# Performance work log

Hardware: AMD Instinct MI355X
Metric: run time of the kernel (lower is better)

Reference implementation:

```python
import jax, jax.numpy as jnp
import numpy as np

B, L, D_IN, D_MODEL, D_OUT, N_LAYERS, N2 = 16, 2048, 512, 512, 512, 4, 32
Q_STEP = 1.0 / 64.0
LN_EPS = 1e-5


def setup_inputs() -> dict:
    key = jax.random.key(0)
    ks = jax.random.split(key, 12)
    H = D_MODEL
    x = jax.random.normal(ks[0], (B, D_IN, L), jnp.float32)
    # sigma-delta dense encoder / decoder weights (ANN-equivalent: dense + ReLU)
    W_enc = jax.random.normal(ks[1], (H, D_IN), jnp.float32) * (1.0 / np.sqrt(D_IN))
    W_dec = jax.random.normal(ks[2], (D_OUT, H), jnp.float32) * (1.0 / np.sqrt(H))
    # S4D kernel params, stacked over layers. S4D-Lin init.
    log_dt = (jax.random.uniform(ks[3], (N_LAYERS, H), jnp.float32)
              * (np.log(0.1) - np.log(0.001)) + np.log(0.001))
    log_A_real = jnp.full((N_LAYERS, H, N2), np.log(0.5), jnp.float32)
    A_imag = jnp.tile((np.pi * jnp.arange(N2, dtype=jnp.float32))[None, None, :],
                      (N_LAYERS, H, 1))
    C_re = jax.random.normal(ks[4], (N_LAYERS, H, N2), jnp.float32) * (0.5 ** 0.5)
    C_im = jax.random.normal(ks[5], (N_LAYERS, H, N2), jnp.float32) * (0.5 ** 0.5)
    D = jax.random.normal(ks[6], (N_LAYERS, H), jnp.float32)
    # output linear of each S4D block: 1x1 conv H -> 2H followed by GLU
    W_out = jax.random.normal(ks[7], (N_LAYERS, 2 * H, H), jnp.float32) * (1.0 / np.sqrt(H))
    b_out = jnp.zeros((N_LAYERS, 2 * H), jnp.float32)
    ln_g = jnp.ones((N_LAYERS, H), jnp.float32)
    ln_b = jnp.zeros((N_LAYERS, H), jnp.float32)
    return {"x": x, "W_enc": W_enc, "W_dec": W_dec, "log_dt": log_dt,
            "log_A_real": log_A_real, "A_imag": A_imag, "C_re": C_re,
            "C_im": C_im, "D": D, "W_out": W_out, "b_out": b_out,
            "ln_g": ln_g, "ln_b": ln_b}


def _quantize_ste(x, step):
    q = jnp.round(x / step) * step
    return x + jax.lax.stop_gradient(q - x)


def reference(x, W_enc, W_dec, log_dt, log_A_real, A_imag, C_re, C_im, D,
              W_out, b_out, ln_g, ln_b):
    # x: (B, d_input, L) channel-time layout (slayer convention)
    xq = _quantize_ste(x, Q_STEP)
    h = jax.nn.relu(jnp.einsum('bct,dc->bdt', xq, W_enc))  # encoder (B,H,L)
    Lx = h.shape[-1]
    t = jnp.arange(Lx)
    for i in range(N_LAYERS):
        # ---- S4D kernel (ZOH-style discretization) ----
        dt = jnp.exp(log_dt[i])[:, None]                 # (H,1)
        A = -jnp.exp(log_A_real[i]) + 1j * A_imag[i]     # (H,N)
        dtA = dt * A                                     # (H,N)
        Cc = (C_re[i] + 1j * C_im[i]) * jnp.expm1(dtA) / A
        vand = jnp.exp(dtA[:, :, None] * t)              # (H,N,L)
        K = 2.0 * jnp.einsum('hn,hnl->hl', Cc, vand).real  # (H,L)
        # ---- FFT convolution ----
        k_f = jnp.fft.rfft(K, n=2 * Lx)                  # (H, L+1)
        u_f = jnp.fft.rfft(h, n=2 * Lx)                  # (B,H,L+1)
        y = jnp.fft.irfft(u_f * k_f[None], n=2 * Lx)[..., :Lx]
        y = y + D[i][:, None] * h                        # skip connection
        y = jax.nn.gelu(y, approximate=False)
        # output linear: 1x1 conv H->2H + GLU over channel dim
        z = jnp.einsum('bht,dh->bdt', y, W_out[i]) + b_out[i][None, :, None]
        z = z[:, :D_MODEL] * jax.nn.sigmoid(z[:, D_MODEL:])
        # residual + post-norm (LayerNorm over channel dim)
        h = z + h
        mu = h.mean(axis=1, keepdims=True)
        var = h.var(axis=1, keepdims=True)
        h = (h - mu) / jnp.sqrt(var + LN_EPS) * ln_g[i][:, None] + ln_b[i][:, None]
    out = jax.nn.relu(jnp.einsum('bht,dh->bdt', h, W_dec))  # decoder (B,d_out,L)
    return out
```

## Files before the change

kernel.cpp:

```cpp
#include <hip/hip_runtime.h>
#include <cstdint>
#include <cstddef>

typedef __attribute__((ext_vector_type(8))) short short8;
typedef __attribute__((ext_vector_type(8))) _Float16 half8;
typedef __attribute__((ext_vector_type(4))) float floatx4;
typedef __attribute__((ext_vector_type(4))) int intx4;
typedef __attribute__((ext_vector_type(4))) unsigned short ushort4v;

__device__ __forceinline__ unsigned short f2h(float f) {
    union { _Float16 h; unsigned short u; } v;
    v.h = (_Float16)f;
    return v.u;
}
__device__ __forceinline__ float relu_keepnan(float v) {
    return v > 0.f ? v : (v == v ? 0.f : v);
}

__global__ __launch_bounds__(256) void k_cvt(
    const float* __restrict__ src, unsigned short* __restrict__ dst, int n) {
    int i = blockIdx.x * 256 + threadIdx.x;
    if (i < n) dst[i] = f2h(src[i]);
}

__global__ __launch_bounds__(256) void k_precompute(
    const float* __restrict__ ldt, const float* __restrict__ lar,
    const float* __restrict__ aim, const float* __restrict__ cre,
    const float* __restrict__ cim, float4* __restrict__ lwc,
    float2* __restrict__ wt) {
    int idx = blockIdx.x * 256 + threadIdx.x;
    int i = idx >> 14;
    int h = (idx >> 5) & 511;
    int n = idx & 31;
    float dt = expf(ldt[i * 512 + h]);
    float Are = -expf(lar[idx]);
    float Aim = aim[idx];
    float dre = dt * Are, dim = dt * Aim;
    float e = expf(dre);
    float wre = e * cosf(dim);
    float wim = e * sinf(dim);
    float emr = wre - 1.f, emi = wim;
    float inv = 1.f / (Are * Are + Aim * Aim);
    float fr = (emr * Are + emi * Aim) * inv;
    float fi = (emi * Are - emr * Aim) * inv;
    float cr = cre[idx], ci = cim[idx];
    float4 o;
    o.x = wre; o.y = wim;
    o.z = 2.f * (cr * fr - ci * fi);
    o.w = 2.f * (cr * fi + ci * fr);
    int oidx = (i * 32 + n) * 512 + h;
    lwc[oidx] = o;
    float ar = wre, ai = wim;
#pragma unroll
    for (int k = 0; k < 7; ++k) {
        float nr = ar * ar - ai * ai;
        float ni = 2.f * ar * ai;
        ar = nr; ai = ni;
    }
    wt[oidx] = make_float2(ar, ai);
}

__global__ __launch_bounds__(256) void k_quant_transpose(
    const float* __restrict__ x, unsigned short* __restrict__ xq, int b0) {
    __shared__ unsigned short tile[64][65];
    const int bg = b0 + blockIdx.z, bl = blockIdx.z;
    const int c0 = blockIdx.y * 64, t0 = blockIdx.x * 64;
    const int tid = threadIdx.x;
#pragma unroll
    for (int it = 0; it < 16; ++it) {
        int idx = it * 256 + tid;
        int r = idx >> 6, cc = idx & 63;
        float f = x[(size_t)(bg * 512 + c0 + r) * 2048 + t0 + cc];
        float q = rintf(f * 64.f) * 0.015625f;
        tile[r][cc] = f2h(q);
    }
    __syncthreads();
#pragma unroll
    for (int it = 0; it < 16; ++it) {
        int idx = it * 256 + tid;
        int r = idx >> 6, cc = idx & 63;
        xq[(size_t)(bl * 2048 + t0 + r) * 512 + c0 + cc] = tile[cc][r];
    }
}

__global__ __launch_bounds__(256) void k_hf2ut(
    const float* __restrict__ hf, unsigned short* __restrict__ ut, int J) {
    __shared__ unsigned short tile[64][65];
    const int j0 = blockIdx.x * 64, c0 = blockIdx.y * 64;
    const int tid = threadIdx.x;
#pragma unroll
    for (int it = 0; it < 16; ++it) {
        int idx = it * 256 + tid;
        int r = idx >> 6, cc = idx & 63;
        tile[r][cc] = f2h(hf[(size_t)(j0 + r) * 512 + c0 + cc]);
    }
    __syncthreads();
#pragma unroll
    for (int it = 0; it < 16; ++it) {
        int idx = it * 256 + tid;
        int r = idx >> 6, cc = idx & 63;
        ut[(size_t)(c0 + r) * J + j0 + cc] = tile[cc][r];
    }
}

__global__ __launch_bounds__(64) void k_build_wa(
    const float4* __restrict__ lwc, unsigned short* __restrict__ WA, int layer) {
    __shared__ unsigned short Ws[64 * 136];
    const int h = blockIdx.x, tid = threadIdx.x;
    if (tid < 32) {
        float4 v = lwc[((size_t)layer * 32 + tid) * 512 + h];
        float pr = 1.f, pi = 0.f;
        for (int m = 0; m < 128; ++m) {
            Ws[(2 * tid) * 136 + (127 - m)] = f2h(pr);
            Ws[(2 * tid + 1) * 136 + (127 - m)] = f2h(pi);
            float nr = pr * v.x - pi * v.y;
            float ni = pr * v.y + pi * v.x;
            pr = nr; pi = ni;
        }
    }
    __syncthreads();
#pragma unroll
    for (int it = 0; it < 16; ++it) {
        int idx = it * 64 + tid;
        int r = idx >> 4, c8 = idx & 15;
        *(intx4*)(WA + (size_t)h * 8192 + r * 128 + c8 * 8) =
            *(const intx4*)(Ws + r * 136 + c8 * 8);
    }
}

__global__ __launch_bounds__(256) void k_build_T(
    const float4* __restrict__ lwc, const float* __restrict__ Dp,
    unsigned short* __restrict__ TT, int layer) {
    __shared__ float Kvs[128];
    __shared__ unsigned short Mxs[128 * 64];
    __shared__ float wr_s[32], wi_s[32], cr_s[32], ci_s[32];
    const int h = blockIdx.x, tid = threadIdx.x;
    if (tid < 32) {
        float4 v = lwc[((size_t)layer * 32 + tid) * 512 + h];
        wr_s[tid] = v.x; wi_s[tid] = v.y; cr_s[tid] = v.z; ci_s[tid] = v.w;
    }
    __syncthreads();
    if (tid < 32) {
        const int n = tid;
        float wre = wr_s[n], wim = wi_s[n];
        float ar = cr_s[n], ai = ci_s[n];
        for (int m = 0; m <= 128; ++m) {
            if (m < 128) {
                float s = ar;
#pragma unroll
                for (int d = 16; d >= 1; d >>= 1) s += __shfl_xor(s, d, 64);
                if (n == 0) Kvs[m] = s;
            }
            if (m >= 1) {
                Mxs[(m - 1) * 64 + 2 * n] = f2h(ar);
                Mxs[(m - 1) * 64 + 2 * n + 1] = f2h(-ai);
            }
            float nr = ar * wre - ai * wim;
            float ni = ar * wim + ai * wre;
            ar = nr; ai = ni;
        }
    }
    __syncthreads();
    const float Dh = Dp[layer * 512 + h];
#pragma unroll
    for (int it = 0; it < 12; ++it) {
        int idx = it * 256 + tid;
        int t = idx / 24, c8 = idx % 24;
        short8 pack;
#pragma unroll
        for (int q = 0; q < 8; ++q) {
            int k = c8 * 8 + q;
            unsigned short us;
            if (k < 128) {
                float val = (k <= t) ? (Kvs[t - k] + (k == t ? Dh : 0.f)) : 0.f;
                us = f2h(val);
            } else {
                us = Mxs[t * 64 + (k - 128)];
            }
            pack[q] = (short)us;
        }
        *(short8*)(TT + (size_t)h * 24576 + t * 192 + c8 * 8) = pack;
    }
}

template <int MODE>
__global__ __launch_bounds__(256, 2) void k_gemm(
    const unsigned short* __restrict__ A, const unsigned short* __restrict__ Bm,
    float* __restrict__ of32, int b0) {
    __shared__ __align__(16) unsigned short Al[128 * 72];
    __shared__ __align__(16) unsigned short Bl[128 * 72];
    const int tid = threadIdx.x;
    const int m0 = blockIdx.x * 128;
    const int j0 = blockIdx.y * 128;
    const int sub = tid & 7;
    const int row = tid >> 3;
    const unsigned short* Ag = A + (size_t)(m0 + row) * 512 + sub * 8;
    const unsigned short* Bg = Bm + (size_t)(j0 + row) * 512 + sub * 8;
    intx4 ra[4], rb[4];
#pragma unroll
    for (int i = 0; i < 4; ++i) {
        ra[i] = *(const intx4*)(Ag + (size_t)i * 32 * 512);
        rb[i] = *(const intx4*)(Bg + (size_t)i * 32 * 512);
    }
    const int lane = tid & 63;
    const int w = tid >> 6;
    const int wm = w & 1, wn = w >> 1;
    const int l15 = lane & 15, quad = lane >> 4;
    floatx4 acc[4][4] = {};
    for (int kt = 0; kt < 8; ++kt) {
#pragma unroll
        for (int i = 0; i < 4; ++i) {
            *(intx4*)(Al + (row + 32 * i) * 72 + sub * 8) = ra[i];
            *(intx4*)(Bl + (row + 32 * i) * 72 + sub * 8) = rb[i];
        }
        __syncthreads();
        if (kt < 7) {
#pragma unroll
            for (int i = 0; i < 4; ++i) {
                ra[i] = *(const intx4*)(Ag + (size_t)i * 32 * 512 + (kt + 1) * 64);
                rb[i] = *(const intx4*)(Bg + (size_t)i * 32 * 512 + (kt + 1) * 64);
            }
        }
#pragma unroll
        for (int ks = 0; ks < 2; ++ks) {
            half8 af[4], bfr[4];
#pragma unroll
            for (int mt = 0; mt < 4; ++mt)
                af[mt] = *(const half8*)(Al + (wm * 64 + mt * 16 + l15) * 72 + ks * 32 + quad * 8);
#pragma unroll
            for (int nt = 0; nt < 4; ++nt)
                bfr[nt] = *(const half8*)(Bl + (wn * 64 + nt * 16 + l15) * 72 + ks * 32 + quad * 8);
#pragma unroll
            for (int mt = 0; mt < 4; ++mt)
#pragma unroll
                for (int nt = 0; nt < 4; ++nt)
                    acc[mt][nt] = __builtin_amdgcn_mfma_f32_16x16x32_f16(
                        af[mt], bfr[nt], acc[mt][nt], 0, 0, 0);
        }
        __syncthreads();
    }
#pragma unroll
    for (int mt = 0; mt < 4; ++mt) {
#pragma unroll
        for (int nt = 0; nt < 4; ++nt) {
            const int d = m0 + wm * 64 + mt * 16 + quad * 4;
            const int j = j0 + wn * 64 + nt * 16 + l15;
            floatx4 v = acc[mt][nt];
            if (MODE == 0) {
#pragma unroll
                for (int r = 0; r < 4; ++r) v[r] = relu_keepnan(v[r]);
                *(floatx4*)(of32 + (size_t)j * 512 + d) = v;
            } else {
                const int bl = j >> 11, t = j & 2047;
#pragma unroll
                for (int r = 0; r < 4; ++r)
                    of32[((size_t)((b0 + bl) * 512 + d + r)) * 2048 + t] = relu_keepnan(v[r]);
            }
        }
    }
}

__global__ __launch_bounds__(256, 4) void k_stateA(
    const unsigned short* __restrict__ WA, const unsigned short* __restrict__ ut,
    float* __restrict__ P, int J, int Rtot) {
    __shared__ __align__(16) unsigned short Aw[64 * 72];
    __shared__ __align__(16) unsigned short Bw[128 * 72];
    const int tid = threadIdx.x;
    const int h = blockIdx.y;
    const int r0 = blockIdx.x * 128;
    const int sub = tid & 7, row = tid >> 3;
    const unsigned short* Ag = WA + (size_t)h * 8192 + row * 128 + sub * 8;
    const unsigned short* Bg = ut + (size_t)h * J + (size_t)(r0 + row) * 128 + sub * 8;
    intx4 ra[2], rb[4];
    ra[0] = *(const intx4*)(Ag);
    ra[1] = *(const intx4*)(Ag + 32 * 128);
#pragma unroll
    for (int i = 0; i < 4; ++i) rb[i] = *(const intx4*)(Bg + i * 32 * 128);
    const int lane = tid & 63, w = tid >> 6;
    const int wm = w & 1, wn = w >> 1;
    const int l15 = lane & 15, quad = lane >> 4;
    floatx4 acc[2][4] = {};
    for (int kt = 0; kt < 2; ++kt) {
        *(intx4*)(Aw + row * 72 + sub * 8) = ra[0];
        *(intx4*)(Aw + (row + 32) * 72 + sub * 8) = ra[1];
#pragma unroll
        for (int i = 0; i < 4; ++i)
            *(intx4*)(Bw + (row + 32 * i) * 72 + sub * 8) = rb[i];
        __syncthreads();
        if (kt == 0) {
            ra[0] = *(const intx4*)(Ag + 64);
            ra[1] = *(const intx4*)(Ag + 32 * 128 + 64);
#pragma unroll
            for (int i = 0; i < 4; ++i) rb[i] = *(const intx4*)(Bg + i * 32 * 128 + 64);
        }
#pragma unroll
        for (int ks = 0; ks < 2; ++ks) {
            half8 af[2], bfr[4];
#pragma unroll
            for (int mt = 0; mt < 2; ++mt)
                af[mt] = *(const half8*)(Aw + (wm * 32 + mt * 16 + l15) * 72 + ks * 32 + quad * 8);
#pragma unroll
            for (int nt = 0; nt < 4; ++nt)
                bfr[nt] = *(const half8*)(Bw + (wn * 64 + nt * 16 + l15) * 72 + ks * 32 + quad * 8);
#pragma unroll
            for (int mt = 0; mt < 2; ++mt)
#pragma unroll
                for (int nt = 0; nt < 4; ++nt)
                    acc[mt][nt] = __builtin_amdgcn_mfma_f32_16x16x32_f16(
                        af[mt], bfr[nt], acc[mt][nt], 0, 0, 0);
        }
        __syncthreads();
    }
#pragma unroll
    for (int mt = 0; mt < 2; ++mt)
#pragma unroll
        for (int nt = 0; nt < 4; ++nt)
#pragma unroll
            for (int r = 0; r < 4; ++r)
                P[((size_t)h * 64 + wm * 32 + mt * 16 + quad * 4 + r) * Rtot +
                  r0 + wn * 64 + nt * 16 + l15] = acc[mt][nt][r];
}

__global__ __launch_bounds__(64) void k_comb(
    const float* __restrict__ P, const float2* __restrict__ wt,
    unsigned short* __restrict__ S0, int layer, int Rtot) {
    __shared__ float Ps[64][17];
    __shared__ unsigned short S0s[16][64];
    const int h = blockIdx.x, bl = blockIdx.y;
    const int tid = threadIdx.x;
#pragma unroll
    for (int it = 0; it < 4; ++it) {
        int idx = it * 64 + tid;
        int n2 = idx >> 2, pt = idx & 3;
        float4 v = *(const float4*)(P + ((size_t)h * 64 + n2) * Rtot + bl * 16 + pt * 4);
        Ps[n2][pt * 4 + 0] = v.x; Ps[n2][pt * 4 + 1] = v.y;
        Ps[n2][pt * 4 + 2] = v.z; Ps[n2][pt * 4 + 3] = v.w;
    }
    __syncthreads();
    if (tid < 32) {
        const int n = tid;
        float2 wv = wt[((size_t)layer * 32 + n) * 512 + h];
        float ar = 0.f, ai = 0.f;
        for (int g = 0; g < 16; ++g) {
            S0s[g][2 * n] = f2h(ar);
            S0s[g][2 * n + 1] = f2h(ai);
            float pr = Ps[2 * n][g], pi = Ps[2 * n + 1][g];
            float nr = fmaf(wv.x, ar, fmaf(-wv.y, ai, pr));
            float ni = fmaf(wv.x, ai, fmaf(wv.y, ar, pi));
            ar = nr; ai = ni;
        }
    }
    __syncthreads();
    const int g = tid >> 2, pt = tid & 3;
    unsigned short* dst = S0 + ((size_t)h * Rtot + bl * 16 + g) * 64 + pt * 16;
    *(intx4*)(dst) = *(const intx4*)(&S0s[g][pt * 16]);
    *(intx4*)(dst + 8) = *(const intx4*)(&S0s[g][pt * 16 + 8]);
}

__global__ __launch_bounds__(256, 2) void k_applyB(
    const unsigned short* __restrict__ TT, const unsigned short* __restrict__ ut,
    const unsigned short* __restrict__ S0, unsigned short* __restrict__ vt,
    int J, int Rtot) {
    __shared__ __align__(16) unsigned short lds[2 * 128 * 72];
    unsigned short* Al = lds;
    unsigned short* Bl = lds + 128 * 72;
    const int tid = threadIdx.x;
    const int h = blockIdx.y;
    const int r0 = blockIdx.x * 128;
    const int sub = tid & 7, row = tid >> 3;
    const unsigned short* Ag = TT + (size_t)h * 24576 + row * 192 + sub * 8;
    const unsigned short* Bu = ut + (size_t)h * J + (size_t)(r0 + row) * 128 + sub * 8;
    const unsigned short* Bs = S0 + ((size_t)h * Rtot + r0 + row) * 64 + sub * 8;
    intx4 ra[4], rb[4];
#pragma unroll
    for (int i = 0; i < 4; ++i) {
        ra[i] = *(const intx4*)(Ag + i * 32 * 192);
        rb[i] = *(const intx4*)(Bu + i * 32 * 128);
    }
    const int lane = tid & 63, w = tid >> 6;
    const int wm = w & 1, wn = w >> 1;
    const int l15 = lane & 15, quad = lane >> 4;
    floatx4 acc[4][4] = {};
    for (int kt = 0; kt < 3; ++kt) {
#pragma unroll
        for (int i = 0; i < 4; ++i) {
            *(intx4*)(Al + (row + 32 * i) * 72 + sub * 8) = ra[i];
            *(intx4*)(Bl + (row + 32 * i) * 72 + sub * 8) = rb[i];
        }
        __syncthreads();
        if (kt == 0) {
#pragma unroll
            for (int i = 0; i < 4; ++i) {
                ra[i] = *(const intx4*)(Ag + i * 32 * 192 + 64);
                rb[i] = *(const intx4*)(Bu + i * 32 * 128 + 64);
            }
        } else if (kt == 1) {
#pragma unroll
            for (int i = 0; i < 4; ++i) {
                ra[i] = *(const intx4*)(Ag + i * 32 * 192 + 128);
                rb[i] = *(const intx4*)(Bs + i * 32 * 64);
            }
        }
#pragma unroll
        for (int ks = 0; ks < 2; ++ks) {
            half8 af[4], bfr[4];
#pragma unroll
            for (int mt = 0; mt < 4; ++mt)
                af[mt] = *(const half8*)(Al + (wm * 64 + mt * 16 + l15) * 72 + ks * 32 + quad * 8);
#pragma unroll
            for (int nt = 0; nt < 4; ++nt)
                bfr[nt] = *(const half8*)(Bl + (wn * 64 + nt * 16 + l15) * 72 + ks * 32 + quad * 8);
#pragma unroll
            for (int mt = 0; mt < 4; ++mt)
#pragma unroll
                for (int nt = 0; nt < 4; ++nt)
                    acc[mt][nt] = __builtin_amdgcn_mfma_f32_16x16x32_f16(
                        af[mt], bfr[nt], acc[mt][nt], 0, 0, 0);
        }
        __syncthreads();
    }
#pragma unroll
    for (int mt = 0; mt < 4; ++mt)
#pragma unroll
        for (int nt = 0; nt < 4; ++nt) {
            const int tl = wm * 64 + mt * 16 + quad * 4;
            const int rl = wn * 64 + nt * 16 + l15;
            ushort4v pack;
#pragma unroll
            for (int r = 0; r < 4; ++r) {
                float y = acc[mt][nt][r];
                float ge = 0.5f * y * (1.f + erff(y * 0.70710678118654752f));
                pack[r] = f2h(ge);
            }
            *(ushort4v*)(lds + rl * 136 + tl) = pack;
        }
    __syncthreads();
    const int rl2 = tid >> 1, hh = tid & 1;
    const unsigned short* srcp = lds + rl2 * 136 + hh * 64;
    unsigned short* dstp = vt + (size_t)h * J + (size_t)(r0 + rl2) * 128 + hh * 64;
#pragma unroll
    for (int q = 0; q < 8; ++q)
        *(intx4*)(dstp + q * 8) = *(const intx4*)(srcp + q * 8);
}

__global__ __launch_bounds__(256, 2) void k_gemm_glu(
    const unsigned short* __restrict__ A,
    const unsigned short* __restrict__ Bt,
    const float* __restrict__ bias,
    float* __restrict__ g_out, int J) {
    __shared__ __align__(16) unsigned short A1l[128 * 72];
    __shared__ __align__(16) unsigned short A2l[128 * 72];
    __shared__ __align__(16) unsigned short Bl[64 * 72];
    const int tid = threadIdx.x;
    const int m0 = blockIdx.x * 128;
    const int j0 = blockIdx.y * 64;
    const int sub = tid & 7;
    const int row = tid >> 3;
    const unsigned short* A1g = A + (size_t)(m0 + row) * 512 + sub * 8;
    const unsigned short* A2g = A1g + 512 * 512;
    const int cB = tid >> 2, jq = tid & 3;
    const unsigned short* Bg = Bt + (size_t)cB * J + j0 + jq * 16;
    intx4 ra1[4], ra2[4], rb0, rb1;
#pragma unroll
    for (int i = 0; i < 4; ++i) {
        ra1[i] = *(const intx4*)(A1g + (size_t)i * 32 * 512);
        ra2[i] = *(const intx4*)(A2g + (size_t)i * 32 * 512);
    }
    rb0 = *(const intx4*)(Bg);
    rb1 = *(const intx4*)(Bg + 8);
    const int lane = tid & 63;
    const int w = tid >> 6;
    const int wm = w & 1, wn = w >> 1;
    const int l15 = lane & 15, quad = lane >> 4;
    floatx4 ac1[4][2] = {}, ac2[4][2] = {};
    for (int kt = 0; kt < 8; ++kt) {
#pragma unroll
        for (int i = 0; i < 4; ++i) {
            *(intx4*)(A1l + (row + 32 * i) * 72 + sub * 8) = ra1[i];
            *(intx4*)(A2l + (row + 32 * i) * 72 + sub * 8) = ra2[i];
        }
#pragma unroll
        for (int ii = 0; ii < 2; ++ii) {
            intx4 rv = ii ? rb1 : rb0;
#pragma unroll
            for (int q = 0; q < 4; ++q) {
                unsigned int w2 = (unsigned int)rv[q];
                Bl[(jq * 16 + ii * 8 + q * 2) * 72 + cB] = (unsigned short)(w2 & 0xffffu);
                Bl[(jq * 16 + ii * 8 + q * 2 + 1) * 72 + cB] = (unsigned short)(w2 >> 16);
            }
        }
        __syncthreads();
        if (kt < 7) {
#pragma unroll
            for (int i = 0; i < 4; ++i) {
                ra1[i] = *(const intx4*)(A1g + (size_t)i * 32 * 512 + (kt + 1) * 64);
                ra2[i] = *(const intx4*)(A2g + (size_t)i * 32 * 512 + (kt + 1) * 64);
            }
            rb0 = *(const intx4*)(Bg + (size_t)(kt + 1) * 64 * J);
            rb1 = *(const intx4*)(Bg + (size_t)(kt + 1) * 64 * J + 8);
        }
#pragma unroll
        for (int ks = 0; ks < 2; ++ks) {
            half8 af1[4], af2[4], bfr[2];
#pragma unroll
            for (int mt = 0; mt < 4; ++mt) {
                af1[mt] = *(const half8*)(A1l + (wm * 64 + mt * 16 + l15) * 72 + ks * 32 + quad * 8);
                af2[mt] = *(const half8*)(A2l + (wm * 64 + mt * 16 + l15) * 72 + ks * 32 + quad * 8);
            }
#pragma unroll
            for (int nt = 0; nt < 2; ++nt)
                bfr[nt] = *(const half8*)(Bl + (wn * 32 + nt * 16 + l15) * 72 + ks * 32 + quad * 8);
#pragma unroll
            for (int mt = 0; mt < 4; ++mt)
#pragma unroll
                for (int nt = 0; nt < 2; ++nt) {
                    ac1[mt][nt] = __builtin_amdgcn_mfma_f32_16x16x32_f16(
                        af1[mt], bfr[nt], ac1[mt][nt], 0, 0, 0);
                    ac2[mt][nt] = __builtin_amdgcn_mfma_f32_16x16x32_f16(
                        af2[mt], bfr[nt], ac2[mt][nt], 0, 0, 0);
                }
        }
        __syncthreads();
    }
#pragma unroll
    for (int mt = 0; mt < 4; ++mt) {
#pragma unroll
        for (int nt = 0; nt < 2; ++nt) {
            const int d = m0 + wm * 64 + mt * 16 + quad * 4;
            const int j = j0 + wn * 32 + nt * 16 + l15;
            floatx4 v;
#pragma unroll
            for (int r = 0; r < 4; ++r) {
                float a = ac1[mt][nt][r] + bias[d + r];
                float gg = ac2[mt][nt][r] + bias[512 + d + r];
                v[r] = a / (1.f + expf(-gg));
            }
            *(floatx4*)(g_out + (size_t)j * 512 + d) = v;
        }
    }
}

__global__ __launch_bounds__(256, 4) void k_res_ln(
    const float* __restrict__ g, float* __restrict__ hf, unsigned short* __restrict__ hb,
    const float* __restrict__ lng, const float* __restrict__ lnb,
    int layer, int wh) {
    __shared__ float r1[4], r2[4];
    const size_t j = blockIdx.x;
    const float* gj = g + j * 512;
    float* hj = hf + j * 512;
    const int tid = threadIdx.x, lane = tid & 63, w = tid >> 6;
    float2 gv = *(const float2*)(gj + tid * 2);
    float2 hv = *(const float2*)(hj + tid * 2);
    float h0 = gv.x + hv.x, h1 = gv.y + hv.y;
    float s1 = h0 + h1, s2 = h0 * h0 + h1 * h1;
#pragma unroll
    for (int m = 32; m >= 1; m >>= 1) { s1 += __shfl_xor(s1, m, 64); s2 += __shfl_xor(s2, m, 64); }
    if (lane == 0) { r1[w] = s1; r2[w] = s2; }
    __syncthreads();
    const float S1 = r1[0] + r1[1] + r1[2] + r1[3];
    const float S2 = r2[0] + r2[1] + r2[2] + r2[3];
    const float mu = S1 * (1.f / 512.f);
    const float var = S2 * (1.f / 512.f) - mu * mu;
    const float isd = 1.f / sqrtf(var + 1e-5f);
    float2 gw = *(const float2*)(lng + layer * 512 + tid * 2);
    float2 bw = *(const float2*)(lnb + layer * 512 + tid * 2);
    float o0 = (h0 - mu) * isd * gw.x + bw.x;
    float o1 = (h1 - mu) * isd * gw.y + bw.y;
    *(float2*)(hj + tid * 2) = make_float2(o0, o1);
    if (wh) *(unsigned int*)(hb + j * 512 + tid * 2) =
        (unsigned int)f2h(o0) | ((unsigned int)f2h(o1) << 16);
}

extern "C" void kernel_launch(void* const* d_in, const int* in_sizes, int n_in,
                              void* d_out, int out_size, void* d_ws, size_t ws_size,
                              hipStream_t stream) {
    (void)in_sizes; (void)n_in; (void)out_size;
    const float* x      = (const float*)d_in[0];
    const float* W_enc  = (const float*)d_in[1];
    const float* W_dec  = (const float*)d_in[2];
    const float* log_dt = (const float*)d_in[3];
    const float* log_Ar = (const float*)d_in[4];
    const float* A_im   = (const float*)d_in[5];
    const float* C_re   = (const float*)d_in[6];
    const float* C_im   = (const float*)d_in[7];
    const float* Dp     = (const float*)d_in[8];
    const float* W_out  = (const float*)d_in[9];
    const float* b_out  = (const float*)d_in[10];
    const float* ln_g   = (const float*)d_in[11];
    const float* ln_b   = (const float*)d_in[12];

    int C = 16;
    while (C > 8 && (size_t)C * (12ull << 20) + (41ull << 20) > ws_size) C >>= 1;
    const size_t J = (size_t)C * 2048;
    const int Rtot = C * 16;

    char* ws = (char*)d_ws;
    size_t off = 0;
    auto alloc = [&](size_t bytes) { void* p = ws + off; off += (bytes + 255) & ~(size_t)255; return p; };
    float4*         lwc   = (float4*)alloc(4ull * 512 * 32 * 16);
    float2*         wt    = (float2*)alloc(4ull * 512 * 32 * 8);
    unsigned short* wencb = (unsigned short*)alloc(512 * 512 * 2);
    unsigned short* wdecb = (unsigned short*)alloc(512 * 512 * 2);
    unsigned short* woutb = (unsigned short*)alloc(4ull * 1024 * 512 * 2);
    unsigned short* WAb   = (unsigned short*)alloc(512ull * 64 * 128 * 2);
    unsigned short* TTb   = (unsigned short*)alloc(512ull * 128 * 192 * 2);
    unsigned short* ut    = (unsigned short*)alloc(512ull * J * 2);
    float*          g     = (float*)alloc(J * 512 * 4);
    float*          hf    = (float*)alloc(J * 512 * 4);
    unsigned short* vt    = (unsigned short*)alloc(J * 512 * 2);
    unsigned short* xq    = (unsigned short*)g;
    unsigned short* hb    = vt;
    float*          P     = (float*)g;
    unsigned short* S0u   = (unsigned short*)((char*)g + (size_t)C * (2ull << 20));

    k_precompute<<<256, 256, 0, stream>>>(log_dt, log_Ar, A_im, C_re, C_im, lwc, wt);
    k_cvt<<<1024, 256, 0, stream>>>(W_enc, wencb, 512 * 512);
    k_cvt<<<1024, 256, 0, stream>>>(W_dec, wdecb, 512 * 512);
    k_cvt<<<8192, 256, 0, stream>>>(W_out, woutb, 4 * 1024 * 512);
    for (int b0 = 0; b0 < 16; b0 += C) {
        k_quant_transpose<<<dim3(32, 8, C), 256, 0, stream>>>(x, xq, b0);
        k_gemm<0><<<dim3(4, C * 16), 256, 0, stream>>>(wencb, xq, hf, 0);
        for (int i = 0; i < 4; ++i) {
            k_build_wa<<<512, 64, 0, stream>>>(lwc, WAb, i);
            k_build_T<<<512, 256, 0, stream>>>(lwc, Dp, TTb, i);
            k_hf2ut<<<dim3(C * 32, 8), 256, 0, stream>>>(hf, ut, (int)J);
            k_stateA<<<dim3(Rtot / 128, 512), 256, 0, stream>>>(WAb, ut, P, (int)J, Rtot);
            k_comb<<<dim3(512, C), 64, 0, stream>>>(P, wt, S0u, i, Rtot);
            k_applyB<<<dim3(Rtot / 128, 512), 256, 0, stream>>>(TTb, ut, S0u, vt, (int)J, Rtot);
            k_gemm_glu<<<dim3(4, C * 32), 256, 0, stream>>>(
                woutb + (size_t)i * 1024 * 512, vt, b_out + (size_t)i * 1024, g, (int)J);
            k_res_ln<<<C * 2048, 256, 0, stream>>>(g, hf, hb, ln_g, ln_b, i, (i == 3) ? 1 : 0);
        }
        k_gemm<2><<<dim3(4, C * 16), 256, 0, stream>>>(wdecb, hb, (float*)d_out, b0);
    }
}
```

Measured before the change: 1.088 ms.

## Swizzle GLU GEMM B-tile LDS stores, swap grid axes, raise occupancy hint

Rewrites how k_gemm_glu loads and transposes the B tile. Each thread now reads two channel rows and packs 32-bit pairs into LDS through an XOR swizzle, replacing scattered 16-bit stores that likely caused bank conflicts. The read side applies the matching swizzle. Both GEMMs also swap their grid axes so consecutive blocks share the same activation column tile, and the GLU kernel's launch bound is raised to 3 waves per SIMD, which may force register spills.

```diff
diff --git a/kernel.cpp b/kernel.cpp
--- a/kernel.cpp
+++ b/kernel.cpp
@@ -190,8 +190,8 @@
     __shared__ __align__(16) unsigned short Al[128 * 72];
     __shared__ __align__(16) unsigned short Bl[128 * 72];
     const int tid = threadIdx.x;
-    const int m0 = blockIdx.x * 128;
-    const int j0 = blockIdx.y * 128;
+    const int m0 = blockIdx.y * 128;
+    const int j0 = blockIdx.x * 128;
     const int sub = tid & 7;
     const int row = tid >> 3;
     const unsigned short* Ag = A + (size_t)(m0 + row) * 512 + sub * 8;
@@ -443,7 +443,7 @@
         *(intx4*)(dstp + q * 8) = *(const intx4*)(srcp + q * 8);
 }
 
-__global__ __launch_bounds__(256, 2) void k_gemm_glu(
+__global__ __launch_bounds__(256, 3) void k_gemm_glu(
     const unsigned short* __restrict__ A,
     const unsigned short* __restrict__ Bt,
     const float* __restrict__ bias,
@@ -452,14 +452,14 @@
     __shared__ __align__(16) unsigned short A2l[128 * 72];
     __shared__ __align__(16) unsigned short Bl[64 * 72];
     const int tid = threadIdx.x;
-    const int m0 = blockIdx.x * 128;
-    const int j0 = blockIdx.y * 64;
+    const int m0 = blockIdx.y * 128;
+    const int j0 = blockIdx.x * 64;
     const int sub = tid & 7;
     const int row = tid >> 3;
     const unsigned short* A1g = A + (size_t)(m0 + row) * 512 + sub * 8;
     const unsigned short* A2g = A1g + 512 * 512;
-    const int cB = tid >> 2, jq = tid & 3;
-    const unsigned short* Bg = Bt + (size_t)cB * J + j0 + jq * 16;
+    const int chp = tid >> 3, jo = tid & 7;
+    const unsigned short* Bg = Bt + (size_t)(2 * chp) * J + j0 + jo * 8;
     intx4 ra1[4], ra2[4], rb0, rb1;
 #pragma unroll
     for (int i = 0; i < 4; ++i) {
@@ -467,11 +467,12 @@
         ra2[i] = *(const intx4*)(A2g + (size_t)i * 32 * 512);
     }
     rb0 = *(const intx4*)(Bg);
-    rb1 = *(const intx4*)(Bg + 8);
+    rb1 = *(const intx4*)(Bg + J);
     const int lane = tid & 63;
     const int w = tid >> 6;
     const int wm = w & 1, wn = w >> 1;
     const int l15 = lane & 15, quad = lane >> 4;
+    const int colbase = (((chp >> 2) ^ jo) << 3) + (chp & 3) * 2;
     floatx4 ac1[4][2] = {}, ac2[4][2] = {};
     for (int kt = 0; kt < 8; ++kt) {
 #pragma unroll
@@ -479,14 +480,15 @@
             *(intx4*)(A1l + (row + 32 * i) * 72 + sub * 8) = ra1[i];
             *(intx4*)(A2l + (row + 32 * i) * 72 + sub * 8) = ra2[i];
         }
-#pragma unroll
-        for (int ii = 0; ii < 2; ++ii) {
-            intx4 rv = ii ? rb1 : rb0;
-#pragma unroll
-            for (int q = 0; q < 4; ++q) {
-                unsigned int w2 = (unsigned int)rv[q];
-                Bl[(jq * 16 + ii * 8 + q * 2) * 72 + cB] = (unsigned short)(w2 & 0xffffu);
-                Bl[(jq * 16 + ii * 8 + q * 2 + 1) * 72 + cB] = (unsigned short)(w2 >> 16);
+        {
+            unsigned int* B32 = (unsigned int*)Bl;
+#pragma unroll
+            for (int i = 0; i < 4; ++i) {
+                unsigned int ae = (unsigned int)rb0[i], be = (unsigned int)rb1[i];
+                unsigned int lo = (ae & 0xffffu) | (be << 16);
+                unsigned int hi = (ae >> 16) | (be & 0xffff0000u);
+                B32[((jo * 8 + 2 * i) * 72 + colbase) >> 1] = lo;
+                B32[((jo * 8 + 2 * i + 1) * 72 + colbase) >> 1] = hi;
             }
         }
         __syncthreads();
@@ -497,7 +499,7 @@
                 ra2[i] = *(const intx4*)(A2g + (size_t)i * 32 * 512 + (kt + 1) * 64);
             }
             rb0 = *(const intx4*)(Bg + (size_t)(kt + 1) * 64 * J);
-            rb1 = *(const intx4*)(Bg + (size_t)(kt + 1) * 64 * J + 8);
+            rb1 = *(const intx4*)(Bg + (size_t)(kt + 1) * 64 * J + J);
         }
 #pragma unroll
         for (int ks = 0; ks < 2; ++ks) {
@@ -508,8 +510,11 @@
                 af2[mt] = *(const half8*)(A2l + (wm * 64 + mt * 16 + l15) * 72 + ks * 32 + quad * 8);
             }
 #pragma unroll
-            for (int nt = 0; nt < 2; ++nt)
-                bfr[nt] = *(const half8*)(Bl + (wn * 32 + nt * 16 + l15) * 72 + ks * 32 + quad * 8);
+            for (int nt = 0; nt < 2; ++nt) {
+                const int rr = wn * 32 + nt * 16 + l15;
+                const int cb = (ks * 4 + quad) ^ (rr >> 3);
+                bfr[nt] = *(const half8*)(Bl + rr * 72 + cb * 8);
+            }
 #pragma unroll
             for (int mt = 0; mt < 4; ++mt)
 #pragma unroll
@@ -619,7 +624,7 @@
     k_cvt<<<8192, 256, 0, stream>>>(W_out, woutb, 4 * 1024 * 512);
     for (int b0 = 0; b0 < 16; b0 += C) {
         k_quant_transpose<<<dim3(32, 8, C), 256, 0, stream>>>(x, xq, b0);
-        k_gemm<0><<<dim3(4, C * 16), 256, 0, stream>>>(wencb, xq, hf, 0);
+        k_gemm<0><<<dim3(C * 16, 4), 256, 0, stream>>>(wencb, xq, hf, 0);
         for (int i = 0; i < 4; ++i) {
             k_build_wa<<<512, 64, 0, stream>>>(lwc, WAb, i);
             k_build_T<<<512, 256, 0, stream>>>(lwc, Dp, TTb, i);
@@ -627,10 +632,10 @@
             k_stateA<<<dim3(Rtot / 128, 512), 256, 0, stream>>>(WAb, ut, P, (int)J, Rtot);
             k_comb<<<dim3(512, C), 64, 0, stream>>>(P, wt, S0u, i, Rtot);
             k_applyB<<<dim3(Rtot / 128, 512), 256, 0, stream>>>(TTb, ut, S0u, vt, (int)J, Rtot);
-            k_gemm_glu<<<dim3(4, C * 32), 256, 0, stream>>>(
+            k_gemm_glu<<<dim3(C * 32, 4), 256, 0, stream>>>(
                 woutb + (size_t)i * 1024 * 512, vt, b_out + (size_t)i * 1024, g, (int)J);
             k_res_ln<<<C * 2048, 256, 0, stream>>>(g, hf, hb, ln_g, ln_b, i, (i == 3) ? 1 : 0);
         }
-        k_gemm<2><<<dim3(4, C * 16), 256, 0, stream>>>(wdecb, hb, (float*)d_out, b0);
-    }
-}
+        k_gemm<2><<<dim3(C * 16, 4), 256, 0, stream>>>(wdecb, hb, (float*)d_out, b0);
+    }
+}
```

Result: faster. 1.057 ms (-2.8%).
